# Kernel tuning notes

Hardware: AMD Instinct MI355X
Metric: run time of the kernel (lower is better)

Reference implementation:

```python
import jax, jax.numpy as jnp
import numpy as np

EMB = 256
HEADS = 4
HD = EMB // HEADS
BS, SZ = 4, 64


def _layernorm(x, g, b, eps=1e-5):
    mu = jnp.mean(x, axis=-1, keepdims=True)
    var = jnp.mean((x - mu) ** 2, axis=-1, keepdims=True)
    return (x - mu) * jax.lax.rsqrt(var + eps) * g + b


def setup_inputs() -> dict:
    key = jax.random.key(0)
    ks = jax.random.split(key, 12)
    s = lambda k, shape, sc: jax.random.normal(k, shape, jnp.float32) * sc
    return {
        "x": s(ks[0], (BS, EMB, SZ, SZ), 1.0),
        "ln1_g": jnp.ones((EMB,), jnp.float32),
        "ln1_b": jnp.zeros((EMB,), jnp.float32),
        "wq": s(ks[1], (HD, HD), HD ** -0.5), "bq": jnp.zeros((HD,), jnp.float32),
        "wk": s(ks[2], (HD, HD), HD ** -0.5), "bk": jnp.zeros((HD,), jnp.float32),
        "wv": s(ks[3], (HD, HD), HD ** -0.5), "bv": jnp.zeros((HD,), jnp.float32),
        "wo": s(ks[4], (EMB, EMB), EMB ** -0.5), "bo": jnp.zeros((EMB,), jnp.float32),
        "ln2_g": jnp.ones((EMB,), jnp.float32),
        "ln2_b": jnp.zeros((EMB,), jnp.float32),
        "w1": s(ks[5], (EMB, EMB), EMB ** -0.5), "b1": jnp.zeros((EMB,), jnp.float32),
        "w2": s(ks[6], (EMB, EMB), EMB ** -0.5), "b2": jnp.zeros((EMB,), jnp.float32),
    }


def reference(x, ln1_g, ln1_b, wq, bq, wk, bk, wv, bv, wo, bo, ln2_g, ln2_b, w1, b1, w2, b2):
    bs, c, sz, _ = x.shape
    seq = sz * sz
    xt = x.reshape(bs, c, seq).swapaxes(1, 2)  # [b, s, c]
    xn = _layernorm(xt, ln1_g, ln1_b)
    # split heads: [b, h, s, d]
    h = xn.reshape(bs, seq, HEADS, HD).transpose(0, 2, 1, 3)
    q = h @ wq + bq
    k = h @ wk + bk
    v = h @ wv + bv
    scores = jnp.einsum("bhqd,bhkd->bhqk", q, k) / (HD ** 0.5)
    attn = jax.nn.softmax(scores, axis=-1)
    o = jnp.einsum("bhqk,bhkd->bhqd", attn, v)
    o = o.transpose(0, 2, 1, 3).reshape(bs, seq, c)
    o = o @ wo + bo
    av = o + xt  # residual 1
    ff = _layernorm(av, ln2_g, ln2_b) @ w1 + b1
    ff = jax.nn.gelu(ff, approximate=False) @ w2 + b2
    out = ff + av  # residual 2
    return out.swapaxes(1, 2).reshape(bs, c, sz, sz)
```

## Files before the change

kernel.cpp:

```cpp
#include <hip/hip_runtime.h>
#include <hip/hip_bf16.h>
#include <cstdint>

typedef __attribute__((ext_vector_type(8))) short short8;
typedef __attribute__((ext_vector_type(4))) short short4_;
typedef __attribute__((ext_vector_type(4))) float float4_;

#define MFMA16(a,b,c)  __builtin_amdgcn_mfma_f32_16x16x32_bf16(a,b,c,0,0,0)
#define MFMA16K16(a,b,c) __builtin_amdgcn_mfma_f32_16x16x16bf16_1k(a,b,c,0,0,0)
#define EXP2(x) __builtin_amdgcn_exp2f(x)

__device__ __forceinline__ short f2bs(float f) {
    union { float f; uint32_t u; } c;
    c.f = f;
    c.u += 0x7FFF + ((c.u >> 16) & 1);
    return (short)(c.u >> 16);
}
__device__ __forceinline__ float s2f(short s) {
    union { uint32_t u; float f; } c;
    c.u = ((uint32_t)(uint16_t)s) << 16;
    return c.f;
}

static const int EMB = 256;
static const int SEQ = 4096;
static const int TOK = 16384;

static const size_t SZO = 4194304;
static const size_t LSTRIDE = 65536;

#define QSCALE 0.18033688011112042f

__global__ __launch_bounds__(256) void repack_kernel(
    const float* wq, const float* wk, const float* wv,
    const float* wo, const float* w1, const float* w2,
    short* wqT, short* wkT, short* wvT, short* woT, short* w1T, short* w2T)
{
    int idx = blockIdx.x * 256 + threadIdx.x;
    if (idx < 3 * 4096) {
        int m = idx / 4096, r = idx % 4096;
        int n = r / 64, k = r % 64;
        const float* src = (m == 0) ? wq : (m == 1) ? wk : wv;
        short* dst = (m == 0) ? wqT : (m == 1) ? wkT : wvT;
        float v = src[k * 64 + n];
        if (m == 0) v *= QSCALE;
        dst[n * 64 + k] = f2bs(v);
    } else {
        int idx2 = idx - 3 * 4096;
        if (idx2 < 3 * 65536) {
            int m = idx2 / 65536, r = idx2 % 65536;
            int n = r / 256, k = r % 256;
            const float* src = (m == 0) ? wo : (m == 1) ? w1 : w2;
            short* dst = (m == 0) ? woT : (m == 1) ? w1T : w2T;
            dst[n * 256 + k] = f2bs(src[k * 256 + n]);
        }
    }
}

__global__ __launch_bounds__(256) void ln1_kernel(
    const float* x, const float* g, const float* bta,
    short* xn, short* xt)
{
    __shared__ float redS[4][32], redQ[4][32];
    int tid = threadIdx.x;
    int l = tid & 31;
    int p = tid >> 5;
    int t = blockIdx.x * 32 + l;
    int b = t >> 12, sp = t & 4095;
    const float* xb = x + (size_t)b * EMB * SEQ + (size_t)(p * 32) * SEQ + sp;

    float v[32];
    float sum = 0.f, ss = 0.f;
#pragma unroll
    for (int j = 0; j < 32; j++) {
        v[j] = xb[(size_t)j * SEQ];
        sum += v[j]; ss += v[j] * v[j];
    }
    sum += __shfl_xor(sum, 32);
    ss  += __shfl_xor(ss, 32);
    int w = tid >> 6;
    if ((tid & 32) == 0) { redS[w][l] = sum; redQ[w][l] = ss; }
    __syncthreads();
    float S = (redS[0][l] + redS[1][l]) + (redS[2][l] + redS[3][l]);
    float Q = (redQ[0][l] + redQ[1][l]) + (redQ[2][l] + redQ[3][l]);
    float mu = S * (1.f / 256.f);
    float var = Q * (1.f / 256.f) - mu * mu;
    float rs = rsqrtf(var + 1e-5f);

    short* xnr = xn + (size_t)t * 256 + p * 32;
    short* xtr = xt + (size_t)t * 256 + p * 32;
#pragma unroll
    for (int c = 0; c < 32; c += 8) {
        short8 ra, na;
#pragma unroll
        for (int j = 0; j < 8; j++) {
            float vv = v[c + j];
            ra[j] = f2bs(vv);
            na[j] = f2bs((vv - mu) * rs * g[p * 32 + c + j] + bta[p * 32 + c + j]);
        }
        *(short8*)(xtr + c) = ra;
        *(short8*)(xnr + c) = na;
    }
}

__global__ __launch_bounds__(256) void qkv_kernel(
    const short* xn, const short* wqT, const short* wkT, const short* wvT,
    const float* bq, const float* bk, const float* bv,
    short* qo, short* ko, short* vto)
{
    int tid = threadIdx.x;
    int w = tid >> 6, lane = tid & 63, quad = lane >> 4, l15 = lane & 15;
    int m0 = blockIdx.x * 64 + w * 16;
    int row = m0 + l15;
    int bb = row >> 12;
    int s0 = (m0 & 4095) + quad * 4;

    short8 a0[4], a1[4];
#pragma unroll
    for (int h = 0; h < 4; h++) {
        a0[h] = *(const short8*)(xn + (size_t)row * 256 + h * 64 + quad * 8);
        a1[h] = *(const short8*)(xn + (size_t)row * 256 + h * 64 + 32 + quad * 8);
    }

#pragma unroll
    for (int p = 0; p < 3; p++) {
        const short* WT = (p == 0) ? wqT : (p == 1) ? wkT : wvT;
        const float* bias = (p == 0) ? bq : (p == 1) ? bk : bv;
        float bscale = (p == 0) ? QSCALE : 1.f;
#pragma unroll
        for (int nb = 0; nb < 4; nb++) {
            int col = nb * 16 + l15;
            short8 b0 = *(const short8*)(WT + col * 64 + quad * 8);
            short8 b1 = *(const short8*)(WT + col * 64 + 32 + quad * 8);
            float bvv = bias[col] * bscale;
#pragma unroll
            for (int h = 0; h < 4; h++) {
                float4_ acc = {bvv, bvv, bvv, bvv};
                acc = MFMA16(a0[h], b0, acc);
                acc = MFMA16(a1[h], b1, acc);
                size_t headbase = (size_t)(bb * 4 + h) * SEQ;
                if (p < 2) {
                    short* dst = (p == 0) ? qo : ko;
#pragma unroll
                    for (int r = 0; r < 4; r++)
                        dst[(headbase + s0 + r) * 64 + col] = f2bs(acc[r]);
                } else {
                    short4_ pk;
#pragma unroll
                    for (int r = 0; r < 4; r++) pk[r] = f2bs(acc[r]);
                    *(short4_*)(vto + ((size_t)(bb * 4 + h) * 64 + col) * SEQ + s0) = pk;
                }
            }
        }
    }
}

__global__ __attribute__((amdgpu_flat_work_group_size(256, 256),
                          amdgpu_waves_per_eu(4, 8)))
void flash_kernel(
    const short* q, const short* k, const short* vt,
    short* O0, short* Orest, float* lbase)
{
    __shared__ short K_lds[64 * 64];
    __shared__ short V_lds[64 * 64];

    int tid = threadIdx.x;
    int w = tid >> 6, lane = tid & 63, quad = lane >> 4, l15 = lane & 15;
    int qt = blockIdx.x, bh = blockIdx.y, grp = blockIdx.z;
    int span = 64 / gridDim.z;

    const short* qb = q + (size_t)bh * SEQ * 64;
    const short* kb = k + (size_t)bh * SEQ * 64 + (size_t)grp * span * 64 * 64;
    const short* vb = vt + (size_t)bh * 64 * SEQ + grp * span * 64;

    int qrow0 = qt * 128 + w * 32 + l15;
    int qrow1 = qrow0 + 16;
    short8 qA0 = *(const short8*)(qb + (size_t)qrow0 * 64 + quad * 8);
    short8 qA1 = *(const short8*)(qb + (size_t)qrow0 * 64 + 32 + quad * 8);
    short8 qB0 = *(const short8*)(qb + (size_t)qrow1 * 64 + quad * 8);
    short8 qB1 = *(const short8*)(qb + (size_t)qrow1 * 64 + 32 + quad * 8);

    float4_ oacc0[4], oacc1[4];
#pragma unroll
    for (int md = 0; md < 4; md++) {
        oacc0[md] = {0.f, 0.f, 0.f, 0.f};
        oacc1[md] = {0.f, 0.f, 0.f, 0.f};
    }
    float li0 = 0.f, li1 = 0.f;

    int srow = tid >> 2;
    int sr7 = srow & 7;
    int c0 = tid & 3;
    int l7 = l15 & 7;

    int dcA = (c0 ^ sr7) << 3;
    int dcB = ((c0 + 4) ^ sr7) << 3;

    short8 kr0 = *(const short8*)(kb + (size_t)srow * 64 + c0 * 8);
    short8 kr1 = *(const short8*)(kb + (size_t)srow * 64 + (c0 + 4) * 8);
    short8 vr0 = *(const short8*)(vb + (size_t)srow * SEQ + c0 * 8);
    short8 vr1 = *(const short8*)(vb + (size_t)srow * SEQ + (c0 + 4) * 8);

    for (int kt = 0; kt < span; kt++) {
        __syncthreads();
        *(short8*)&K_lds[srow * 64 + dcA] = kr0;
        *(short8*)&K_lds[srow * 64 + dcB] = kr1;
        *(short8*)&V_lds[srow * 64 + dcA] = vr0;
        *(short8*)&V_lds[srow * 64 + dcB] = vr1;
        if (kt + 1 < span) {
            kr0 = *(const short8*)(kb + (size_t)((kt + 1) * 64 + srow) * 64 + c0 * 8);
            kr1 = *(const short8*)(kb + (size_t)((kt + 1) * 64 + srow) * 64 + (c0 + 4) * 8);
            vr0 = *(const short8*)(vb + (size_t)srow * SEQ + (kt + 1) * 64 + c0 * 8);
            vr1 = *(const short8*)(vb + (size_t)srow * SEQ + (kt + 1) * 64 + (c0 + 4) * 8);
        }
        asm volatile("s_waitcnt lgkmcnt(0)" ::: "memory");
        __builtin_amdgcn_s_barrier();
        asm volatile("" ::: "memory");

        short4_ pf0[4], pf1[4];
#pragma unroll
        for (int nb = 0; nb < 4; nb++) {
            short8 k0 = *(const short8*)&K_lds[(nb * 16 + l15) * 64 + ((quad ^ l7) << 3)];
            short8 k1 = *(const short8*)&K_lds[(nb * 16 + l15) * 64 + (((quad + 4) ^ l7) << 3)];
            float4_ a = {0.f, 0.f, 0.f, 0.f};
            a = MFMA16(k0, qA0, a);
            a = MFMA16(k1, qA1, a);
            float4_ b = {0.f, 0.f, 0.f, 0.f};
            b = MFMA16(k0, qB0, b);
            b = MFMA16(k1, qB1, b);

            float p00 = EXP2(a[0]), p01 = EXP2(a[1]);
            float p02 = EXP2(a[2]), p03 = EXP2(a[3]);
            li0 += (p00 + p01) + (p02 + p03);
            float p10 = EXP2(b[0]), p11 = EXP2(b[1]);
            float p12 = EXP2(b[2]), p13 = EXP2(b[3]);
            li1 += (p10 + p11) + (p12 + p13);
            union { short4_ s; uint32_t u[2]; } pa, pb;
            asm("v_cvt_pk_bf16_f32 %0, %1, %2" : "=v"(pa.u[0]) : "v"(p00), "v"(p01));
            asm("v_cvt_pk_bf16_f32 %0, %1, %2" : "=v"(pa.u[1]) : "v"(p02), "v"(p03));
            asm("v_cvt_pk_bf16_f32 %0, %1, %2" : "=v"(pb.u[0]) : "v"(p10), "v"(p11));
            asm("v_cvt_pk_bf16_f32 %0, %1, %2" : "=v"(pb.u[1]) : "v"(p12), "v"(p13));
            pf0[nb] = pa.s;
            pf1[nb] = pb.s;
        }

        __builtin_amdgcn_s_setprio(1);
#pragma unroll
        for (int md = 0; md < 4; md++)
#pragma unroll
            for (int nb = 0; nb < 4; nb++) {
                int c = nb * 2 + (quad >> 1);
                short4_ vf = *(const short4_*)&V_lds[(md * 16 + l15) * 64 +
                                                     ((c ^ l7) << 3) + ((quad & 1) << 2)];
                oacc0[md] = MFMA16K16(vf, pf0[nb], oacc0[md]);
                oacc1[md] = MFMA16K16(vf, pf1[nb], oacc1[md]);
            }
        __builtin_amdgcn_s_setprio(0);
    }

    li0 += __shfl_xor(li0, 16);
    li0 += __shfl_xor(li0, 32);
    li1 += __shfl_xor(li1, 16);
    li1 += __shfl_xor(li1, 32);

    short* Op = grp ? (Orest + (size_t)(grp - 1) * SZO) : O0;
    float* lp = lbase + (size_t)grp * LSTRIDE;
    if (quad == 0) {
        lp[bh * 4096 + qrow0] = li0;
        lp[bh * 4096 + qrow1] = li1;
    }

    size_t ob0 = ((size_t)bh * 4096 + qrow0) * 64;
    size_t ob1 = ((size_t)bh * 4096 + qrow1) * 64;
#pragma unroll
    for (int md = 0; md < 4; md++) {
        short4_ pk0, pk1;
#pragma unroll
        for (int r = 0; r < 4; r++) {
            pk0[r] = f2bs(oacc0[md][r]);
            pk1[r] = f2bs(oacc1[md][r]);
        }
        *(short4_*)(Op + ob0 + md * 16 + quad * 4) = pk0;
        *(short4_*)(Op + ob1 + md * 16 + quad * 4) = pk1;
    }
}

__global__ __launch_bounds__(256) void combine_kernel(
    const short* O0, const short* Orest, const float* lb,
    short* Oout, int np)
{
    int g = blockIdx.x * 256 + threadIdx.x;
    int qi = g >> 4;
    short4_ a = *(const short4_*)(O0 + (size_t)g * 4);
    float l = lb[qi];
    float4_ acc = {s2f(a[0]), s2f(a[1]), s2f(a[2]), s2f(a[3])};
    for (int j = 1; j < np; j++) {
        short4_ b = *(const short4_*)(Orest + (size_t)(j - 1) * SZO + (size_t)g * 4);
        l += lb[(size_t)j * LSTRIDE + qi];
#pragma unroll
        for (int jj = 0; jj < 4; jj++) acc[jj] += s2f(b[jj]);
    }
    float inv = 1.f / l;
    short4_ pk;
#pragma unroll
    for (int j = 0; j < 4; j++) pk[j] = f2bs(acc[j] * inv);
    *(short4_*)(Oout + (size_t)g * 4) = pk;
}

__global__ __launch_bounds__(256) void mlp_kernel(
    const short* O0, const short* Orest, const float* lb, int np,
    const short* woT, const short* w1T, const short* w2T,
    const float* bo, const float* b1, const float* b2,
    const float* g2, const float* be2,
    const short* xt, float* outf)
{
    __shared__ __align__(16) char smem[3 * 8448 + 128];
    short* av = (short*)smem;
    short* x2 = (short*)(smem + 8448);
    short* ff = (short*)(smem + 16896);
    float* stats = (float*)(smem + 25344);
    float* T = (float*)smem;

    int tid = threadIdx.x;
    int w = tid >> 6, lane = tid & 63, quad = lane >> 4, l15 = lane & 15;
    int m0 = blockIdx.x * 16;
    int n0 = w * 64;
    int arow = m0 + l15;
    int bbA = arow >> 12, spA = arow & 4095;

    float invh[4];
    if (np) {
#pragma unroll
        for (int h = 0; h < 4; h++) {
            size_t li = (size_t)(bbA * 4 + h) * 4096 + spA;
            float s = lb[li];
            for (int j = 1; j < np; j++) s += lb[(size_t)j * LSTRIDE + li];
            invh[h] = 1.f / s;
        }
    }

    float4_ acc[4];
#pragma unroll
    for (int nb = 0; nb < 4; nb++) {
        float bvv = bo[n0 + nb * 16 + l15];
        acc[nb] = {bvv, bvv, bvv, bvv};
    }
    for (int kc = 0; kc < 8; kc++) {
        int h = kc >> 1;
        int off = (kc & 1) * 32 + quad * 8;
        size_t obase = ((size_t)(bbA * 4 + h) * 4096 + spA) * 64 + off;
        short8 a;
        if (np) {
            short8 a0v = *(const short8*)(O0 + obase);
            float f[8];
#pragma unroll
            for (int jj = 0; jj < 8; jj++) f[jj] = s2f(a0v[jj]);
            for (int j = 1; j < np; j++) {
                short8 apv = *(const short8*)(Orest + (size_t)(j - 1) * SZO + obase);
#pragma unroll
                for (int jj = 0; jj < 8; jj++) f[jj] += s2f(apv[jj]);
            }
            float iv = invh[h];
            union { short8 s; uint32_t u[4]; } pa;
#pragma unroll
            for (int jj = 0; jj < 4; jj++) {
                float f0 = f[2 * jj] * iv;
                float f1 = f[2 * jj + 1] * iv;
                asm("v_cvt_pk_bf16_f32 %0, %1, %2" : "=v"(pa.u[jj]) : "v"(f0), "v"(f1));
            }
            a = pa.s;
        } else {
            a = *(const short8*)(O0 + obase);
        }
#pragma unroll
        for (int nb = 0; nb < 4; nb++) {
            short8 b = *(const short8*)(woT + (size_t)(n0 + nb * 16 + l15) * 256 + kc * 32 + quad * 8);
            acc[nb] = MFMA16(a, b, acc[nb]);
        }
    }
#pragma unroll
    for (int nb = 0; nb < 4; nb++) {
        int col = n0 + nb * 16 + l15;
#pragma unroll
        for (int r = 0; r < 4; r++) {
            size_t t = (size_t)m0 + quad * 4 + r;
            av[(quad * 4 + r) * 264 + col] = f2bs(acc[nb][r] + s2f(xt[t * 256 + col]));
        }
    }
    __syncthreads();

    {
        int row = tid >> 4, sub = tid & 15;
        float sum = 0.f, ss = 0.f;
        short8 v0 = *(const short8*)&av[row * 264 + sub * 16];
        short8 v1 = *(const short8*)&av[row * 264 + sub * 16 + 8];
#pragma unroll
        for (int j = 0; j < 8; j++) {
            float a = s2f(v0[j]), b = s2f(v1[j]);
            sum += a + b; ss += a * a + b * b;
        }
#pragma unroll
        for (int off = 1; off < 16; off <<= 1) {
            sum += __shfl_xor(sum, off);
            ss += __shfl_xor(ss, off);
        }
        if (sub == 0) {
            float mu = sum * (1.f / 256.f);
            float var = ss * (1.f / 256.f) - mu * mu;
            stats[row] = mu;
            stats[16 + row] = rsqrtf(var + 1e-5f);
        }
    }
    __syncthreads();

    {
        int row = tid >> 4, sub = tid & 15;
        float mu = stats[row], rs = stats[16 + row];
#pragma unroll
        for (int j = 0; j < 16; j += 4) {
            int c = sub * 16 + j;
            short4_ rv = *(const short4_*)&av[row * 264 + c];
            short4_ pk;
#pragma unroll
            for (int i = 0; i < 4; i++)
                pk[i] = f2bs((s2f(rv[i]) - mu) * rs * g2[c + i] + be2[c + i]);
            *(short4_*)&x2[row * 264 + c] = pk;
        }
    }
    __syncthreads();

#pragma unroll
    for (int nb = 0; nb < 4; nb++) {
        float bvv = b1[n0 + nb * 16 + l15];
        acc[nb] = {bvv, bvv, bvv, bvv};
    }
    for (int kc = 0; kc < 8; kc++) {
        short8 a = *(const short8*)&x2[l15 * 264 + kc * 32 + quad * 8];
#pragma unroll
        for (int nb = 0; nb < 4; nb++) {
            short8 b = *(const short8*)(w1T + (size_t)(n0 + nb * 16 + l15) * 256 + kc * 32 + quad * 8);
            acc[nb] = MFMA16(a, b, acc[nb]);
        }
    }
#pragma unroll
    for (int nb = 0; nb < 4; nb++) {
        int col = n0 + nb * 16 + l15;
#pragma unroll
        for (int r = 0; r < 4; r++) {
            float v = acc[nb][r];
            v = 0.5f * v * (1.f + erff(v * 0.70710678118f));
            ff[(quad * 4 + r) * 264 + col] = f2bs(v);
        }
    }
    __syncthreads();

#pragma unroll
    for (int nb = 0; nb < 4; nb++) {
        float bvv = b2[n0 + nb * 16 + l15];
        acc[nb] = {bvv, bvv, bvv, bvv};
    }
    for (int kc = 0; kc < 8; kc++) {
        short8 a = *(const short8*)&ff[l15 * 264 + kc * 32 + quad * 8];
#pragma unroll
        for (int nb = 0; nb < 4; nb++) {
            short8 b = *(const short8*)(w2T + (size_t)(n0 + nb * 16 + l15) * 256 + kc * 32 + quad * 8);
            acc[nb] = MFMA16(a, b, acc[nb]);
        }
    }
    float vout[4][4];
#pragma unroll
    for (int nb = 0; nb < 4; nb++) {
        int col = n0 + nb * 16 + l15;
#pragma unroll
        for (int r = 0; r < 4; r++)
            vout[nb][r] = acc[nb][r] + s2f(av[(quad * 4 + r) * 264 + col]);
    }
    __syncthreads();

    float* tw = T + w * 1040;
#pragma unroll
    for (int nb = 0; nb < 4; nb++)
#pragma unroll
        for (int r = 0; r < 4; r++)
            tw[(quad * 4 + r) * 65 + nb * 16 + l15] = vout[nb][r];

    int bb = m0 >> 12;
    int spb = m0 & 4095;
    float* dst = outf + ((size_t)bb * 256 + n0 + lane) * SEQ + spb;
#pragma unroll
    for (int j = 0; j < 16; j += 4) {
        float4_ pk = {tw[(j + 0) * 65 + lane], tw[(j + 1) * 65 + lane],
                      tw[(j + 2) * 65 + lane], tw[(j + 3) * 65 + lane]};
        *(float4_*)(dst + j) = pk;
    }
}

extern "C" void kernel_launch(void* const* d_in, const int* in_sizes, int n_in,
                              void* d_out, int out_size, void* d_ws, size_t ws_size,
                              hipStream_t stream)
{
    const float* x     = (const float*)d_in[0];
    const float* ln1_g = (const float*)d_in[1];
    const float* ln1_b = (const float*)d_in[2];
    const float* wq    = (const float*)d_in[3];
    const float* bq    = (const float*)d_in[4];
    const float* wk    = (const float*)d_in[5];
    const float* bk    = (const float*)d_in[6];
    const float* wv    = (const float*)d_in[7];
    const float* bv    = (const float*)d_in[8];
    const float* wo    = (const float*)d_in[9];
    const float* bo    = (const float*)d_in[10];
    const float* ln2_g = (const float*)d_in[11];
    const float* ln2_b = (const float*)d_in[12];
    const float* w1    = (const float*)d_in[13];
    const float* b1    = (const float*)d_in[14];
    const float* w2    = (const float*)d_in[15];
    const float* b2    = (const float*)d_in[16];

    char* ws = (char*)d_ws;
    const size_t SZ_BF = (size_t)TOK * 256 * 2;

    short* wqT = (short*)(ws + 0);
    short* wkT = (short*)(ws + 8192);
    short* wvT = (short*)(ws + 16384);
    short* woT = (short*)(ws + 24576);
    short* w1T = (short*)(ws + 155648);
    short* w2T = (short*)(ws + 286720);
    char* base = ws + 524288;

    short* xt  = (short*)(base);
    short* kbuf= (short*)(base + SZ_BF);
    short* vtb = (short*)(base + 2 * SZ_BF);

    const size_t need2_fb = 524288 + 3 * SZ_BF + 524288 + SZ_BF;
    const size_t need2_fu = need2_fb + SZ_BF;
    const size_t need4_fb = 524288 + 3 * SZ_BF + 1048576 + 3 * SZ_BF;
    const size_t need4_fu = need4_fb + SZ_BF;

    int nz, fuse;
    if (ws_size >= need4_fb)      { nz = 4; fuse = (ws_size >= need4_fu); }
    else if (ws_size >= need2_fb) { nz = 2; fuse = (ws_size >= need2_fu); }
    else                          { nz = 1; fuse = 0; }

    float* lbase;
    short* Orest;
    short* O0w;
    if (nz == 4) {
        lbase = (float*)(base + 3 * SZ_BF);
        Orest = (short*)(base + 3 * SZ_BF + 1048576);
        O0w   = Orest + 3 * SZO;
    } else {
        lbase = (float*)(base + 3 * SZ_BF);
        Orest = (short*)(base + 3 * SZ_BF + 524288);
        O0w   = Orest + SZO;
    }

    short* qb  = (short*)d_out;
    short* xn  = (short*)((char*)d_out + SZ_BF);
    short* O0  = fuse ? O0w : xn;
    short* Onrm= vtb;

    repack_kernel<<<816, 256, 0, stream>>>(wq, wk, wv, wo, w1, w2,
                                           wqT, wkT, wvT, woT, w1T, w2T);
    ln1_kernel<<<TOK / 32, 256, 0, stream>>>(x, ln1_g, ln1_b, xn, xt);
    qkv_kernel<<<TOK / 64, 256, 0, stream>>>(xn, wqT, wkT, wvT, bq, bk, bv,
                                             qb, kbuf, vtb);
    flash_kernel<<<dim3(32, 16, nz), 256, 0, stream>>>(qb, kbuf, vtb, O0, Orest, lbase);
    if (fuse) {
        mlp_kernel<<<TOK / 16, 256, 0, stream>>>(O0, Orest, lbase, nz,
                                                 woT, w1T, w2T, bo, b1, b2,
                                                 ln2_g, ln2_b, xt, (float*)d_out);
    } else {
        combine_kernel<<<4096, 256, 0, stream>>>(O0, Orest, lbase, Onrm, nz);
        mlp_kernel<<<TOK / 16, 256, 0, stream>>>(Onrm, Orest, lbase, 0,
                                                 woT, w1T, w2T, bo, b1, b2,
                                                 ln2_g, ln2_b, xt, (float*)d_out);
    }
}
```

Measured before the change: 271.5 us.

## Switch flash attention inner loop to 32x32x16 MFMA with permlane swap

Rewrites the flash attention kernel's QK^T and PV products to use 32x32x16 bf16 MFMA tiles instead of 16x16 tiles. Each wave now owns 32 query rows in one lane group, with P fragments rearranged through v_permlane32_swap rather than the K16 MFMA path. The goal is fewer MFMA issues and LDS reads per tile plus a cheaper row-sum reduction. In exchange it uses larger accumulators, which raises register pressure, and it pins waves_per_eu to 4.

```diff
diff --git a/kernel.cpp b/kernel.cpp
--- a/kernel.cpp
+++ b/kernel.cpp
@@ -5,9 +5,10 @@
 typedef __attribute__((ext_vector_type(8))) short short8;
 typedef __attribute__((ext_vector_type(4))) short short4_;
 typedef __attribute__((ext_vector_type(4))) float float4_;
+typedef __attribute__((ext_vector_type(16))) float f32x16;
 
 #define MFMA16(a,b,c)  __builtin_amdgcn_mfma_f32_16x16x32_bf16(a,b,c,0,0,0)
-#define MFMA16K16(a,b,c) __builtin_amdgcn_mfma_f32_16x16x16bf16_1k(a,b,c,0,0,0)
+#define MFMA32(a,b,c)  __builtin_amdgcn_mfma_f32_32x32x16_bf16(a,b,c,0,0,0)
 #define EXP2(x) __builtin_amdgcn_exp2f(x)
 
 __device__ __forceinline__ short f2bs(float f) {
@@ -156,7 +157,7 @@
 }
 
 __global__ __attribute__((amdgpu_flat_work_group_size(256, 256),
-                          amdgpu_waves_per_eu(4, 8)))
+                          amdgpu_waves_per_eu(4, 4)))
 void flash_kernel(
     const short* q, const short* k, const short* vt,
     short* O0, short* Orest, float* lbase)
@@ -165,7 +166,8 @@
     __shared__ short V_lds[64 * 64];
 
     int tid = threadIdx.x;
-    int w = tid >> 6, lane = tid & 63, quad = lane >> 4, l15 = lane & 15;
+    int w = tid >> 6, lane = tid & 63;
+    int l31 = lane & 31, hh = lane >> 5, l7 = l31 & 7;
     int qt = blockIdx.x, bh = blockIdx.y, grp = blockIdx.z;
     int span = 64 / gridDim.z;
 
@@ -173,26 +175,22 @@
     const short* kb = k + (size_t)bh * SEQ * 64 + (size_t)grp * span * 64 * 64;
     const short* vb = vt + (size_t)bh * 64 * SEQ + grp * span * 64;
 
-    int qrow0 = qt * 128 + w * 32 + l15;
-    int qrow1 = qrow0 + 16;
-    short8 qA0 = *(const short8*)(qb + (size_t)qrow0 * 64 + quad * 8);
-    short8 qA1 = *(const short8*)(qb + (size_t)qrow0 * 64 + 32 + quad * 8);
-    short8 qB0 = *(const short8*)(qb + (size_t)qrow1 * 64 + quad * 8);
-    short8 qB1 = *(const short8*)(qb + (size_t)qrow1 * 64 + 32 + quad * 8);
-
-    float4_ oacc0[4], oacc1[4];
-#pragma unroll
-    for (int md = 0; md < 4; md++) {
-        oacc0[md] = {0.f, 0.f, 0.f, 0.f};
-        oacc1[md] = {0.f, 0.f, 0.f, 0.f};
-    }
-    float li0 = 0.f, li1 = 0.f;
+    int qrow = qt * 128 + w * 32 + l31;
+    short8 qf[4];
+#pragma unroll
+    for (int kb4 = 0; kb4 < 4; kb4++)
+        qf[kb4] = *(const short8*)(qb + (size_t)qrow * 64 + kb4 * 16 + hh * 8);
+
+    f32x16 oacc[2];
+#pragma unroll
+    for (int td = 0; td < 2; td++)
+#pragma unroll
+        for (int i = 0; i < 16; i++) oacc[td][i] = 0.f;
+    float li = 0.f;
 
     int srow = tid >> 2;
     int sr7 = srow & 7;
     int c0 = tid & 3;
-    int l7 = l15 & 7;
-
     int dcA = (c0 ^ sr7) << 3;
     int dcB = ((c0 + 4) ^ sr7) << 3;
 
@@ -217,72 +215,72 @@
         __builtin_amdgcn_s_barrier();
         asm volatile("" ::: "memory");
 
-        short4_ pf0[4], pf1[4];
-#pragma unroll
-        for (int nb = 0; nb < 4; nb++) {
-            short8 k0 = *(const short8*)&K_lds[(nb * 16 + l15) * 64 + ((quad ^ l7) << 3)];
-            short8 k1 = *(const short8*)&K_lds[(nb * 16 + l15) * 64 + (((quad + 4) ^ l7) << 3)];
-            float4_ a = {0.f, 0.f, 0.f, 0.f};
-            a = MFMA16(k0, qA0, a);
-            a = MFMA16(k1, qA1, a);
-            float4_ b = {0.f, 0.f, 0.f, 0.f};
-            b = MFMA16(k0, qB0, b);
-            b = MFMA16(k1, qB1, b);
-
-            float p00 = EXP2(a[0]), p01 = EXP2(a[1]);
-            float p02 = EXP2(a[2]), p03 = EXP2(a[3]);
-            li0 += (p00 + p01) + (p02 + p03);
-            float p10 = EXP2(b[0]), p11 = EXP2(b[1]);
-            float p12 = EXP2(b[2]), p13 = EXP2(b[3]);
-            li1 += (p10 + p11) + (p12 + p13);
-            union { short4_ s; uint32_t u[2]; } pa, pb;
-            asm("v_cvt_pk_bf16_f32 %0, %1, %2" : "=v"(pa.u[0]) : "v"(p00), "v"(p01));
-            asm("v_cvt_pk_bf16_f32 %0, %1, %2" : "=v"(pa.u[1]) : "v"(p02), "v"(p03));
-            asm("v_cvt_pk_bf16_f32 %0, %1, %2" : "=v"(pb.u[0]) : "v"(p10), "v"(p11));
-            asm("v_cvt_pk_bf16_f32 %0, %1, %2" : "=v"(pb.u[1]) : "v"(p12), "v"(p13));
-            pf0[nb] = pa.s;
-            pf1[nb] = pb.s;
-        }
-
-        __builtin_amdgcn_s_setprio(1);
-#pragma unroll
-        for (int md = 0; md < 4; md++)
-#pragma unroll
-            for (int nb = 0; nb < 4; nb++) {
-                int c = nb * 2 + (quad >> 1);
-                short4_ vf = *(const short4_*)&V_lds[(md * 16 + l15) * 64 +
-                                                     ((c ^ l7) << 3) + ((quad & 1) << 2)];
-                oacc0[md] = MFMA16K16(vf, pf0[nb], oacc0[md]);
-                oacc1[md] = MFMA16K16(vf, pf1[nb], oacc1[md]);
+#pragma unroll
+        for (int t = 0; t < 2; t++) {
+            f32x16 acc;
+#pragma unroll
+            for (int i = 0; i < 16; i++) acc[i] = 0.f;
+#pragma unroll
+            for (int kb4 = 0; kb4 < 4; kb4++) {
+                short8 ka = *(const short8*)&K_lds[(t * 32 + l31) * 64 +
+                                                   (((kb4 * 2 + hh) ^ l7) << 3)];
+                acc = MFMA32(ka, qf[kb4], acc);
             }
-        __builtin_amdgcn_s_setprio(0);
-    }
-
-    li0 += __shfl_xor(li0, 16);
-    li0 += __shfl_xor(li0, 32);
-    li1 += __shfl_xor(li1, 16);
-    li1 += __shfl_xor(li1, 32);
+#pragma unroll
+            for (int i = 0; i < 16; i++) acc[i] = EXP2(acc[i]);
+            li += ((acc[0] + acc[1]) + (acc[2] + acc[3]))
+                + ((acc[4] + acc[5]) + (acc[6] + acc[7]))
+                + ((acc[8] + acc[9]) + (acc[10] + acc[11]))
+                + ((acc[12] + acc[13]) + (acc[14] + acc[15]));
+            short8 wf[2];
+#pragma unroll
+            for (int kbl = 0; kbl < 2; kbl++) {
+                uint32_t A0, A1, B0, B1;
+                asm("v_cvt_pk_bf16_f32 %0, %1, %2" : "=v"(A0)
+                    : "v"(acc[kbl * 8 + 0]), "v"(acc[kbl * 8 + 1]));
+                asm("v_cvt_pk_bf16_f32 %0, %1, %2" : "=v"(A1)
+                    : "v"(acc[kbl * 8 + 2]), "v"(acc[kbl * 8 + 3]));
+                asm("v_cvt_pk_bf16_f32 %0, %1, %2" : "=v"(B0)
+                    : "v"(acc[kbl * 8 + 4]), "v"(acc[kbl * 8 + 5]));
+                asm("v_cvt_pk_bf16_f32 %0, %1, %2" : "=v"(B1)
+                    : "v"(acc[kbl * 8 + 6]), "v"(acc[kbl * 8 + 7]));
+                asm("v_permlane32_swap_b32 %0, %1" : "+v"(A0), "+v"(B0));
+                asm("v_permlane32_swap_b32 %0, %1" : "+v"(A1), "+v"(B1));
+                union { short8 s; uint32_t u[4]; } pw;
+                pw.u[0] = A0; pw.u[1] = A1; pw.u[2] = B0; pw.u[3] = B1;
+                wf[kbl] = pw.s;
+            }
+            __builtin_amdgcn_s_setprio(1);
+#pragma unroll
+            for (int kbl = 0; kbl < 2; kbl++) {
+                int kc = (t * 2 + kbl) * 2 + hh;
+#pragma unroll
+                for (int td = 0; td < 2; td++) {
+                    short8 va = *(const short8*)&V_lds[(td * 32 + l31) * 64 +
+                                                       ((kc ^ l7) << 3)];
+                    oacc[td] = MFMA32(va, wf[kbl], oacc[td]);
+                }
+            }
+            __builtin_amdgcn_s_setprio(0);
+        }
+    }
+
+    li += __shfl_xor(li, 32);
 
     short* Op = grp ? (Orest + (size_t)(grp - 1) * SZO) : O0;
     float* lp = lbase + (size_t)grp * LSTRIDE;
-    if (quad == 0) {
-        lp[bh * 4096 + qrow0] = li0;
-        lp[bh * 4096 + qrow1] = li1;
-    }
-
-    size_t ob0 = ((size_t)bh * 4096 + qrow0) * 64;
-    size_t ob1 = ((size_t)bh * 4096 + qrow1) * 64;
-#pragma unroll
-    for (int md = 0; md < 4; md++) {
-        short4_ pk0, pk1;
-#pragma unroll
-        for (int r = 0; r < 4; r++) {
-            pk0[r] = f2bs(oacc0[md][r]);
-            pk1[r] = f2bs(oacc1[md][r]);
-        }
-        *(short4_*)(Op + ob0 + md * 16 + quad * 4) = pk0;
-        *(short4_*)(Op + ob1 + md * 16 + quad * 4) = pk1;
-    }
+    if (hh == 0) lp[bh * 4096 + qrow] = li;
+
+    size_t ob = ((size_t)bh * 4096 + qrow) * 64;
+#pragma unroll
+    for (int td = 0; td < 2; td++)
+#pragma unroll
+        for (int g = 0; g < 4; g++) {
+            short4_ pk;
+#pragma unroll
+            for (int r = 0; r < 4; r++) pk[r] = f2bs(oacc[td][g * 4 + r]);
+            *(short4_*)(Op + ob + td * 32 + g * 8 + hh * 4) = pk;
+        }
 }
 
 __global__ __launch_bounds__(256) void combine_kernel(
```

Measured after the change: 298.0 us. +9.8%, slower.
